# Performance work log

Measured on AMD Instinct MI355X. Metric: run time of the kernel, lower is better.

Reference implementation:

```python
import jax, jax.numpy as jnp
import numpy as np

K = 3
STRIDE = 1
PADDING = 1


def _conv2d(x, w, b, stride, padding):
    out = jax.lax.conv_general_dilated(
        x, w, window_strides=(stride, stride),
        padding=[(padding, padding), (padding, padding)],
        dimension_numbers=('NCHW', 'OIHW', 'NCHW'))
    return out + b[None, :, None, None]


def _grid_sample_bilinear_zeros(x, grid):
    B, C, Hin, Win = x.shape
    gx = (grid[..., 0] + 1.0) * (Win * 0.5) - 0.5  # (B,Hg,Wg) pixel coords
    gy = (grid[..., 1] + 1.0) * (Hin * 0.5) - 0.5
    x0f = jnp.floor(gx)
    y0f = jnp.floor(gy)
    wx1 = gx - x0f  # bilinear weights
    wy1 = gy - y0f
    x0 = x0f.astype(jnp.int32)
    y0 = y0f.astype(jnp.int32)
    xf = x.reshape(B, C, Hin * Win)

    def gather(yi, xi):
        valid = (xi >= 0) & (xi < Win) & (yi >= 0) & (yi < Hin)  # zero padding
        idx = jnp.clip(yi, 0, Hin - 1) * Win + jnp.clip(xi, 0, Win - 1)
        g = jax.vmap(lambda xb, ib: xb[:, ib])(xf, idx)  # (B,C,Hg,Wg)
        return g * valid[:, None, :, :].astype(x.dtype)

    w00 = ((1.0 - wx1) * (1.0 - wy1))[:, None]
    w01 = (wx1 * (1.0 - wy1))[:, None]
    w10 = ((1.0 - wx1) * wy1)[:, None]
    w11 = (wx1 * wy1)[:, None]
    return (gather(y0, x0) * w00 + gather(y0, x0 + 1) * w01 +
            gather(y0 + 1, x0) * w10 + gather(y0 + 1, x0 + 1) * w11)


def setup_inputs() -> dict:
    key = jax.random.key(0)
    k1, k2, k3 = jax.random.split(key, 3)
    B, C, O, H, W = 8, 128, 128, 64, 64
    x = jax.random.normal(k1, (B, C, H, W), dtype=jnp.float32)
    # small offset-predictor weights so sampled locations stay near the grid
    w_off = jax.random.normal(k2, (2 * K * K, C, K, K), dtype=jnp.float32) * 1e-3
    b_off = jnp.zeros((2 * K * K,), dtype=jnp.float32)
    w_main = jax.random.normal(k3, (O, C, K, K), dtype=jnp.float32) * 0.05
    b_main = jnp.zeros((O,), dtype=jnp.float32)
    return {"x": x, "w_off": w_off, "b_off": b_off, "w_main": w_main, "b_main": b_main}


def reference(x, w_off, b_off, w_main, b_main):
    offset = _conv2d(x, w_off, b_off, STRIDE, PADDING)  # (B, 2*K*K, H, W)
    B, _, H, W = offset.shape
    off = jnp.transpose(offset, (0, 2, 3, 1)).reshape(B, H, W, K, K, 2)
    # The torch in-place loops reduce to:
    #   x-comp: cumsum over i of column j=0, broadcast over j
    #   y-comp: cumsum over j of row    i=0, broadcast over i
    ox = jnp.cumsum(off[:, :, :, :, 0, 0], axis=3)  # (B,H,W,K)
    oy = jnp.cumsum(off[:, :, :, 0, :, 1], axis=3)  # (B,H,W,K)
    ox_f = jnp.broadcast_to(ox[..., None], (B, H, W, K, K))
    oy_f = jnp.broadcast_to(oy[:, :, :, None, :], (B, H, W, K, K))
    off_f = jnp.stack([ox_f, oy_f], axis=-1).reshape(B, H, W, K * K, 2)

    y_range = jnp.linspace(-1.0, 1.0, H, dtype=x.dtype)
    x_range = jnp.linspace(-1.0, 1.0, W, dtype=x.dtype)
    yg, xg = jnp.meshgrid(y_range, x_range, indexing='ij')
    base = jnp.stack((xg, yg), axis=-1)  # (H,W,2)
    grid = base[None, :, :, None, :] + off_f  # (B,H,W,K*K,2)
    grid = grid.reshape(B, H, W * K * K, 2)

    xs = _grid_sample_bilinear_zeros(x, grid)  # (B,C,H,W*K*K)
    C = x.shape[1]
    xs = xs.reshape(B, C, H, W, K * K)
    wm = w_main.reshape(w_main.shape[0], C, K * K)
    out = jnp.einsum('bchwk,ock->bohw', xs, wm)
    return out + b_main[None, :, None, None]
```

## Files before the change

kernel.cpp:

```cpp
#include <hip/hip_runtime.h>
#include <hip/hip_bf16.h>
#include <stdint.h>

typedef unsigned short u16;
typedef unsigned int u32;
typedef __attribute__((ext_vector_type(8))) short short8;
typedef __attribute__((ext_vector_type(4))) float float4v;
typedef __attribute__((ext_vector_type(2))) float float2v;

#define CH 128
#define OO 128
#define KD 1152
#define MPIX 32768

__device__ __forceinline__ u16 f2bf(float v) {
    __hip_bfloat16 h = __float2bfloat16(v);
    return *reinterpret_cast<u16*>(&h);
}

__device__ __forceinline__ float bf_lo(u32 u) {
    u32 t = u << 16;
    return __builtin_bit_cast(float, t);
}
__device__ __forceinline__ float bf_hi(u32 u) {
    u32 t = u & 0xffff0000u;
    return __builtin_bit_cast(float, t);
}
__device__ __forceinline__ float2v unpk(u32 u) {
    float2v r;
    r.x = bf_lo(u);
    r.y = bf_hi(u);
    return r;
}
__device__ __forceinline__ u32 pack_bf16(float lo, float hi) {
    u32 ul = __builtin_bit_cast(u32, lo);
    u32 uh = __builtin_bit_cast(u32, hi);
    return ((ul + 0x8000u) >> 16) | ((uh + 0x8000u) & 0xffff0000u);
}

__global__ __launch_bounds__(256) void prep_kernel(const float* __restrict__ x,
                                                   const float* __restrict__ w_off,
                                                   const float* __restrict__ w_main,
                                                   __hip_bfloat16* __restrict__ xt,
                                                   float* __restrict__ partial,
                                                   u16* __restrict__ Wb) {
    __shared__ float st[64][65];
    int tid = threadIdx.x;
    int bid = blockIdx.x;

    if (bid < 512) {
        int bh = bid;
        int b = bh >> 6;
        int h = bh & 63;
        const float* xb = x + ((size_t)b * CH) * 4096 + (size_t)h * 64;
        __hip_bfloat16* xo = xt + ((size_t)bh << 6) * CH;
        for (int cc0 = 0; cc0 < 128; cc0 += 64) {
            #pragma unroll
            for (int step = 0; step < 16; ++step) {
                int cl = (tid >> 6) + step * 4;
                int w = tid & 63;
                st[cl][w] = xb[(size_t)(cc0 + cl) * 4096 + w];
            }
            __syncthreads();
            #pragma unroll
            for (int step = 0; step < 16; ++step) {
                int w = (tid >> 6) + step * 4;
                int cl = tid & 63;
                xo[(size_t)w * CH + cc0 + cl] = __float2bfloat16(st[cl][w]);
            }
            __syncthreads();
        }
    } else if (bid < 1024) {
        int idx = bid - 512;
        int m = (idx & 127) * 256 + tid;
        int chunk = idx >> 7;
        int b = m >> 12;
        int hw = m & 4095;
        int h = hw >> 6;
        int w = hw & 63;
        float acc[6] = {0.f, 0.f, 0.f, 0.f, 0.f, 0.f};
        int c0 = chunk * 32;
        for (int c = c0; c < c0 + 32; ++c) {
            const float* xc = x + ((size_t)(b * CH + c) << 12);
            float xv[9];
            #pragma unroll
            for (int dy = 0; dy < 3; ++dy) {
                int yy = h + dy - 1;
                bool vy = (unsigned)yy < 64u;
                #pragma unroll
                for (int dx = 0; dx < 3; ++dx) {
                    int xx = w + dx - 1;
                    bool vv = vy && ((unsigned)xx < 64u);
                    xv[dy * 3 + dx] = vv ? xc[yy * 64 + xx] : 0.f;
                }
            }
            const float* wb = w_off + (size_t)c * 9;
            #pragma unroll
            for (int s = 0; s < 6; ++s) {
                int chn = (s < 3) ? s * 6 : (s - 3) * 2 + 1;
                const float* wp = wb + (size_t)chn * (CH * 9);
                float a = acc[s];
                #pragma unroll
                for (int t = 0; t < 9; ++t) a = fmaf(xv[t], wp[t], a);
                acc[s] = a;
            }
        }
        float* po = partial + ((size_t)(chunk << 15) + m) * 6;
        #pragma unroll
        for (int s = 0; s < 6; ++s) po[s] = acc[s];
    } else {
        int idx = (bid - 1024) * 256 + tid;
        if (idx < OO * KD) {
            int o = idx / KD;
            int r = idx - o * KD;
            int k = r >> 7;
            int c = r & 127;
            Wb[idx] = f2bf(w_main[(size_t)o * KD + c * 9 + k]);
        }
    }
}

__global__ __launch_bounds__(256) void fused_gemm_kernel(const __hip_bfloat16* __restrict__ xt,
                                                         const float* __restrict__ partial,
                                                         const float* __restrict__ b_off,
                                                         const u16* __restrict__ Wb,
                                                         const float* __restrict__ b_main,
                                                         float* __restrict__ out) {
    __shared__ float offs[64][6];
    __shared__ __align__(16) float4v twt[64][9];
    __shared__ __align__(16) int4 tbs[64][9];
    __shared__ __align__(16) u16 lA[2][128 * 32];
    __shared__ __align__(16) u16 lB[2][64 * 32];

    int tid = threadIdx.x;
    int orig = blockIdx.x;
    int b = orig & 7;
    int h = orig >> 3;
    int m0 = ((b << 6) + h) << 6;

    for (int idx = tid; idx < 64 * 6; idx += 256) {
        int pix = idx / 6, s = idx % 6;
        int m = m0 + pix;
        int chn = (s < 3) ? s * 6 : (s - 3) * 2 + 1;
        float v = b_off[chn];
        #pragma unroll
        for (int q = 0; q < 4; ++q) v += partial[((size_t)(q << 15) + m) * 6 + s];
        offs[pix][s] = v;
    }
    __syncthreads();

    for (int idx = tid; idx < 64 * 9; idx += 256) {
        int pix = idx / 9, k = idx % 9;
        int i = k / 3, j = k - i * 3;
        float ox = offs[pix][0];
        if (i >= 1) ox += offs[pix][1];
        if (i >= 2) ox += offs[pix][2];
        float oy = offs[pix][3];
        if (j >= 1) oy += offs[pix][4];
        if (j >= 2) oy += offs[pix][5];
        const float step = 2.0f / 63.0f;
        float bxn = -1.0f + pix * step;
        float byn = -1.0f + h * step;
        float gx = fmaf(bxn + ox, 32.0f, 31.5f);
        float gy = fmaf(byn + oy, 32.0f, 31.5f);
        float x0f = floorf(gx), y0f = floorf(gy);
        float wx = gx - x0f, wy = gy - y0f;
        int ix0 = (int)x0f, iy0 = (int)y0f;
        int ix1 = ix0 + 1, iy1 = iy0 + 1;
        float fx0 = ((unsigned)ix0 < 64u) ? 1.f : 0.f;
        float fx1 = ((unsigned)ix1 < 64u) ? 1.f : 0.f;
        float fy0 = ((unsigned)iy0 < 64u) ? 1.f : 0.f;
        float fy1 = ((unsigned)iy1 < 64u) ? 1.f : 0.f;
        float4v wv;
        wv[0] = (1.f - wy) * (1.f - wx) * fy0 * fx0;
        wv[1] = (1.f - wy) * wx * fy0 * fx1;
        wv[2] = wy * (1.f - wx) * fy1 * fx0;
        wv[3] = wy * wx * fy1 * fx1;
        int cx0 = min(max(ix0, 0), 63), cx1 = min(max(ix1, 0), 63);
        int cy0 = min(max(iy0, 0), 63), cy1 = min(max(iy1, 0), 63);
        twt[pix][k] = wv;
        tbs[pix][k] = make_int4((cy0 * 64 + cx0) * 64, (cy0 * 64 + cx1) * 64,
                                (cy1 * 64 + cx0) * 64, (cy1 * 64 + cx1) * 64);
    }
    __syncthreads();

    int wave = tid >> 6, lane = tid & 63;
    int wo = wave & 1;
    int wp = wave >> 1;
    int mrow = lane & 15;
    int q8 = (lane >> 4) * 8;

    int pix = tid >> 2;
    int cg = (tid & 3) * 8;
    const u32* xb = (const u32*)(xt + (((size_t)b << 12) * (size_t)CH));
    const u16* abase = Wb + (size_t)(tid >> 2) * KD + (tid & 3) * 8;
    int asto = (tid >> 2) * 32 + (tid & 3) * 8;
    int bsto = pix * 32 + cg;

    float4v acc[4][2];
    #pragma unroll
    for (int sm = 0; sm < 4; ++sm)
        #pragma unroll
        for (int sn = 0; sn < 2; ++sn)
            acc[sm][sn] = (float4v){0.f, 0.f, 0.f, 0.f};

    float4v wv;
    int4 bv;
    uint4 u00, u01, u10, u11, a0, a1;

    auto issue = [&](int kk) {
        if ((kk & 3) == 0) {
            int k = kk >> 2;
            wv = twt[pix][k];
            bv = tbs[pix][k];
        }
        const u32* xc = xb + ((((kk & 3) << 5) + cg) >> 1);
        u00 = *(const uint4*)(xc + bv.x);
        u01 = *(const uint4*)(xc + bv.y);
        u10 = *(const uint4*)(xc + bv.z);
        u11 = *(const uint4*)(xc + bv.w);
        const u16* ap = abase + kk * 32;
        a0 = *(const uint4*)ap;
        a1 = *(const uint4*)(ap + (size_t)64 * KD);
    };

    issue(0);

    for (int kk = 0; kk < 36; ++kk) {
        int cur = kk & 1;
        u16* lAc = &lA[cur][0];
        u16* lBc = &lB[cur][0];

        *(uint4*)&lAc[asto] = a0;
        *(uint4*)&lAc[asto + 64 * 32] = a1;
        {
            const u32* p00 = (const u32*)&u00;
            const u32* p01 = (const u32*)&u01;
            const u32* p10 = (const u32*)&u10;
            const u32* p11 = (const u32*)&u11;
            u32 outp[4];
            #pragma unroll
            for (int q = 0; q < 4; ++q) {
                float2v p = unpk(p00[q]) * wv[0];
                p += unpk(p01[q]) * wv[1];
                p += unpk(p10[q]) * wv[2];
                p += unpk(p11[q]) * wv[3];
                outp[q] = pack_bf16(p.x, p.y);
            }
            *(uint4*)&lBc[bsto] = *(const uint4*)outp;
        }

        if (kk < 35) issue(kk + 1);

        __syncthreads();

        short8 af[4], bfv[2];
        #pragma unroll
        for (int s = 0; s < 4; ++s)
            af[s] = *(const short8*)&lAc[(wo * 64 + s * 16 + mrow) * 32 + q8];
        #pragma unroll
        for (int s = 0; s < 2; ++s)
            bfv[s] = *(const short8*)&lBc[(wp * 32 + s * 16 + mrow) * 32 + q8];
        #pragma unroll
        for (int sm = 0; sm < 4; ++sm)
            #pragma unroll
            for (int sn = 0; sn < 2; ++sn)
                acc[sm][sn] = __builtin_amdgcn_mfma_f32_16x16x32_bf16(af[sm], bfv[sn],
                                                                     acc[sm][sn], 0, 0, 0);
    }

    #pragma unroll
    for (int sm = 0; sm < 4; ++sm) {
        int o = wo * 64 + sm * 16 + (lane >> 4) * 4;
        #pragma unroll
        for (int sn = 0; sn < 2; ++sn) {
            int pcol = m0 + wp * 32 + sn * 16 + mrow;
            int rem = pcol & 4095;
            float* op = out + (((size_t)b * OO) << 12) + rem;
            #pragma unroll
            for (int r = 0; r < 4; ++r)
                op[(size_t)(o + r) << 12] = acc[sm][sn][r] + b_main[o + r];
        }
    }
}

extern "C" void kernel_launch(void* const* d_in, const int* in_sizes, int n_in,
                              void* d_out, int out_size, void* d_ws, size_t ws_size,
                              hipStream_t stream) {
    const float* x      = (const float*)d_in[0];
    const float* w_off  = (const float*)d_in[1];
    const float* b_off  = (const float*)d_in[2];
    const float* w_main = (const float*)d_in[3];
    const float* b_main = (const float*)d_in[4];
    float* out = (float*)d_out;

    char* ws = (char*)d_ws;
    __hip_bfloat16* xt = (__hip_bfloat16*)ws;
    float* partial = (float*)(ws + 8388608);
    u16* Wb   = (u16*)(ws + 8388608 + 3145728);

    prep_kernel<<<1600, 256, 0, stream>>>(x, w_off, w_main, xt, partial, Wb);
    fused_gemm_kernel<<<MPIX / 64, 256, 0, stream>>>(xt, partial, b_off, Wb, b_main, out);
}
```

Baseline: 129.3 us.

## Load GEMM weight fragments directly into registers, skipping LDS staging

The main GEMM kernel no longer stages weight (A) tiles through shared memory. Each wave now loads its MFMA A fragments straight from global memory into double-buffered registers, which removes the LDS writes and reads for A and shrinks shared-memory use. The prep transpose now writes packed bf16 pairs as 32-bit stores, and the bf16 packing uses the library conversion. In exchange, the weight loads become redundant across waves and each thread holds more registers.

```diff
diff --git a/kernel.cpp b/kernel.cpp
--- a/kernel.cpp
+++ b/kernel.cpp
@@ -33,9 +33,7 @@
     return r;
 }
 __device__ __forceinline__ u32 pack_bf16(float lo, float hi) {
-    u32 ul = __builtin_bit_cast(u32, lo);
-    u32 uh = __builtin_bit_cast(u32, hi);
-    return ((ul + 0x8000u) >> 16) | ((uh + 0x8000u) & 0xffff0000u);
+    return (u32)f2bf(lo) | ((u32)f2bf(hi) << 16);
 }
 
 __global__ __launch_bounds__(256) void prep_kernel(const float* __restrict__ x,
@@ -53,7 +51,7 @@
         int b = bh >> 6;
         int h = bh & 63;
         const float* xb = x + ((size_t)b * CH) * 4096 + (size_t)h * 64;
-        __hip_bfloat16* xo = xt + ((size_t)bh << 6) * CH;
+        u32* xo32 = (u32*)(xt + ((size_t)bh << 6) * CH);
         for (int cc0 = 0; cc0 < 128; cc0 += 64) {
             #pragma unroll
             for (int step = 0; step < 16; ++step) {
@@ -63,10 +61,11 @@
             }
             __syncthreads();
             #pragma unroll
-            for (int step = 0; step < 16; ++step) {
-                int w = (tid >> 6) + step * 4;
-                int cl = tid & 63;
-                xo[(size_t)w * CH + cc0 + cl] = __float2bfloat16(st[cl][w]);
+            for (int step = 0; step < 8; ++step) {
+                int w = (tid >> 5) + step * 8;
+                int p = tid & 31;
+                u32 pair = pack_bf16(st[2 * p][w], st[2 * p + 1][w]);
+                xo32[(size_t)w * 64 + (cc0 >> 1) + p] = pair;
             }
             __syncthreads();
         }
@@ -129,7 +128,6 @@
     __shared__ float offs[64][6];
     __shared__ __align__(16) float4v twt[64][9];
     __shared__ __align__(16) int4 tbs[64][9];
-    __shared__ __align__(16) u16 lA[2][128 * 32];
     __shared__ __align__(16) u16 lB[2][64 * 32];
 
     int tid = threadIdx.x;
@@ -191,11 +189,10 @@
     int q8 = (lane >> 4) * 8;
 
     int pix = tid >> 2;
-    int cg = (tid & 3) * 8;
+    int cgp = (tid & 3) * 8;
     const u32* xb = (const u32*)(xt + (((size_t)b << 12) * (size_t)CH));
-    const u16* abase = Wb + (size_t)(tid >> 2) * KD + (tid & 3) * 8;
-    int asto = (tid >> 2) * 32 + (tid & 3) * 8;
-    int bsto = pix * 32 + cg;
+    const u16* arow = Wb + (size_t)(wo * 64 + mrow) * KD + q8;
+    int bsto = pix * 32 + cgp;
 
     float4v acc[4][2];
     #pragma unroll
@@ -206,33 +203,29 @@
 
     float4v wv;
     int4 bv;
-    uint4 u00, u01, u10, u11, a0, a1;
-
-    auto issue = [&](int kk) {
+    uint4 u00, u01, u10, u11;
+
+    auto issueB = [&](int kk) {
         if ((kk & 3) == 0) {
             int k = kk >> 2;
             wv = twt[pix][k];
             bv = tbs[pix][k];
         }
-        const u32* xc = xb + ((((kk & 3) << 5) + cg) >> 1);
+        const u32* xc = xb + ((((kk & 3) << 5) + cgp) >> 1);
         u00 = *(const uint4*)(xc + bv.x);
         u01 = *(const uint4*)(xc + bv.y);
         u10 = *(const uint4*)(xc + bv.z);
         u11 = *(const uint4*)(xc + bv.w);
-        const u16* ap = abase + kk * 32;
-        a0 = *(const uint4*)ap;
-        a1 = *(const uint4*)(ap + (size_t)64 * KD);
     };
-
-    issue(0);
-
-    for (int kk = 0; kk < 36; ++kk) {
-        int cur = kk & 1;
-        u16* lAc = &lA[cur][0];
-        u16* lBc = &lB[cur][0];
-
-        *(uint4*)&lAc[asto] = a0;
-        *(uint4*)&lAc[asto + 64 * 32] = a1;
+    auto issueA = [&](int kk, uint4* dst) {
+        const u16* ap = arow + kk * 32;
+        #pragma unroll
+        for (int s = 0; s < 4; ++s)
+            dst[s] = *(const uint4*)(ap + (size_t)(s * 16) * KD);
+    };
+
+    auto dostep = [&](int kk, uint4* aC, uint4* aN) {
+        u16* lBc = &lB[kk & 1][0];
         {
             const u32* p00 = (const u32*)&u00;
             const u32* p01 = (const u32*)&u01;
@@ -250,23 +243,33 @@
             *(uint4*)&lBc[bsto] = *(const uint4*)outp;
         }
 
-        if (kk < 35) issue(kk + 1);
+        if (kk < 35) {
+            issueB(kk + 1);
+            issueA(kk + 1, aN);
+        }
 
         __syncthreads();
 
-        short8 af[4], bfv[2];
-        #pragma unroll
-        for (int s = 0; s < 4; ++s)
-            af[s] = *(const short8*)&lAc[(wo * 64 + s * 16 + mrow) * 32 + q8];
+        short8 bfv[2];
         #pragma unroll
         for (int s = 0; s < 2; ++s)
             bfv[s] = *(const short8*)&lBc[(wp * 32 + s * 16 + mrow) * 32 + q8];
         #pragma unroll
-        for (int sm = 0; sm < 4; ++sm)
+        for (int sm = 0; sm < 4; ++sm) {
+            short8 af = __builtin_bit_cast(short8, aC[sm]);
             #pragma unroll
             for (int sn = 0; sn < 2; ++sn)
-                acc[sm][sn] = __builtin_amdgcn_mfma_f32_16x16x32_bf16(af[sm], bfv[sn],
+                acc[sm][sn] = __builtin_amdgcn_mfma_f32_16x16x32_bf16(af, bfv[sn],
                                                                      acc[sm][sn], 0, 0, 0);
+        }
+    };
+
+    uint4 aP[4], aQ[4];
+    issueB(0);
+    issueA(0, aP);
+    for (int t = 0; t < 18; ++t) {
+        dostep(2 * t, aP, aQ);
+        dostep(2 * t + 1, aQ, aP);
     }
 
     #pragma unroll
```

Result: slower. 143.0 us (+10.6%).
